# Kernel optimization log

Hardware: AMD Instinct MI355X
Metric: run time of the kernel (lower is better)

## Reference

```python
import jax, jax.numpy as jnp
import numpy as np

H = 4096      # hidden_size
Hk = 16       # num_key_heads
Dk = 256      # key_head_dim
Hv = 32       # num_value_heads
Dv = 256      # value_head_dim
G = 2         # kv_group_size
Ve = 512      # value_expand = G*Dv
CS = 4        # conv_size
QK = Hk * Dk  # 4096
VD = Hv * Dv  # 8192
EPS = 1e-6


def setup_inputs() -> dict:
    key = jax.random.key(0)
    ks = jax.random.split(key, 14)
    n = lambda i, shape, s: jax.random.normal(ks[i], shape, jnp.float32) * s
    return {
        "hidden_states": n(0, (1, H, 1, 1), 1.0),
        "Wq": n(1, (QK, H), 0.02),
        "Wk": n(2, (QK, H), 0.02),
        "Wv": n(3, (VD, H), 0.02),
        "Wo": n(4, (H, VD), 0.02),
        "Wa": n(5, (Hk, H), 0.02),
        "Wb": n(6, (Hk, H), 0.02),
        "q_conv_w": n(7, (1, QK, CS), 0.5),
        "k_conv_w": n(8, (1, QK, CS), 0.5),
        "v_conv_w": n(9, (1, VD, CS), 0.5),
        "q_cache": n(10, (1, QK, CS - 1), 1.0),
        "k_cache": n(11, (1, QK, CS - 1), 1.0),
        "v_cache": n(12, (1, VD, CS - 1), 1.0),
        "state": n(13, (1, Hk, Dk, Ve), 0.1),
    }


def _l2norm(x):
    return x * jax.lax.rsqrt(jnp.sum(x * x, axis=-1, keepdims=True) + EPS)


def reference(hidden_states, Wq, Wk, Wv, Wo, Wa, Wb,
              q_conv_w, k_conv_w, v_conv_w,
              q_cache, k_cache, v_cache, state):
    h = hidden_states[0, :, 0, 0]  # [H]
    q = Wq @ h                      # [QK]
    k = Wk @ h                      # [QK]
    v = Wv @ h                      # [VD]
    alpha = jax.nn.sigmoid(Wa @ h)  # [Hk]
    beta = jax.nn.sigmoid(Wb @ h)   # [Hk]

    # depthwise causal conv via cache concat + mul-sum, then SiLU
    q_full = jnp.concatenate([q_cache, q[None, :, None]], axis=2)  # [1,QK,CS]
    k_full = jnp.concatenate([k_cache, k[None, :, None]], axis=2)
    v_full = jnp.concatenate([v_cache, v[None, :, None]], axis=2)  # [1,VD,CS]
    q1 = jax.nn.silu(jnp.sum(q_full * q_conv_w, axis=2))  # [1,QK]
    k1 = jax.nn.silu(jnp.sum(k_full * k_conv_w, axis=2))
    v1 = jax.nn.silu(jnp.sum(v_full * v_conv_w, axis=2))  # [1,VD]

    q_heads = _l2norm(q1.reshape(1, Hk, Dk))
    k_heads = _l2norm(k1.reshape(1, Hk, Dk))
    v_heads = v1.reshape(1, Hk, Ve)  # Hv=Hk*G, Ve=G*Dv

    a = alpha.reshape(1, Hk, 1, 1)
    b = beta.reshape(1, Hk, 1, 1)
    state_decayed = state * a                                   # [1,Hk,Dk,Ve]
    retrieved = jnp.einsum('bhdv,bhd->bhv', state_decayed, k_heads)
    error = v_heads - retrieved                                 # [1,Hk,Ve]
    outer = k_heads[..., None] * error[:, :, None, :]           # [1,Hk,Dk,Ve]
    new_state = state_decayed + b * outer
    out = jnp.einsum('bhdv,bhd->bhv', new_state, q_heads)       # [1,Hk,Ve]
    out = out.reshape(1, VD)
    output = (out @ Wo.T).reshape(1, H, 1, 1)
    return output
```

## Files before the change

kernel.cpp:

```cpp
#include <hip/hip_runtime.h>
#include <math.h>

#define HDIM 4096
#define HK 16
#define DK 256
#define VE 512
#define QK 4096
#define VD 8192
#define NCHUNK 16
#define DPC 16
#define EPS 1e-6f

#define OFF_Q    0
#define OFF_K    4096
#define OFF_V    8192
#define OFF_AB   16384
#define OFF_KQ   16416
#define OFF_OUT  16432
#define OFF_PQ   24624
#define OFF_PK   (24624 + NCHUNK*VD)

typedef float f4_t __attribute__((ext_vector_type(4)));

__device__ __forceinline__ float sigmoidf_(float x) { return 1.f / (1.f + __expf(-x)); }
__device__ __forceinline__ float siluf_(float x)    { return x / (1.f + __expf(-x)); }

__global__ __launch_bounds__(256) void k1_gemv_all(
    const float* __restrict__ hvec,
    const float* __restrict__ Wq, const float* __restrict__ Wk,
    const float* __restrict__ Wv, const float* __restrict__ Wa,
    const float* __restrict__ Wb, float* __restrict__ ws) {
  int tid = threadIdx.x;
  int wave = tid >> 6, lane = tid & 63;
  int row = blockIdx.x * 4 + wave;
  if (row >= 16416) return;

  const f4_t* w4; float* outp;
  if (row < 4096)       { w4 = (const f4_t*)(Wq + (size_t)row * HDIM);            outp = ws + OFF_Q + row; }
  else if (row < 8192)  { int r = row - 4096;  w4 = (const f4_t*)(Wk + (size_t)r * HDIM); outp = ws + OFF_K + r; }
  else if (row < 16384) { int r = row - 8192;  w4 = (const f4_t*)(Wv + (size_t)r * HDIM); outp = ws + OFF_V + r; }
  else if (row < 16400) { int r = row - 16384; w4 = (const f4_t*)(Wa + (size_t)r * HDIM); outp = ws + OFF_AB + r; }
  else                  { int r = row - 16400; w4 = (const f4_t*)(Wb + (size_t)r * HDIM); outp = ws + OFF_AB + 16 + r; }

  const f4_t* h4 = (const f4_t*)hvec;
  float acc = 0.f;
#pragma unroll
  for (int j = 0; j < 16; ++j) {
    f4_t w  = __builtin_nontemporal_load(&w4[j * 64 + lane]);
    f4_t hv = h4[j * 64 + lane];
    acc += w.x * hv.x + w.y * hv.y + w.z * hv.z + w.w * hv.w;
  }
#pragma unroll
  for (int off = 32; off; off >>= 1) acc += __shfl_xor(acc, off, 64);
  if (lane == 0) *outp = acc;
}

__global__ __launch_bounds__(512) void kB_state(
    const float* __restrict__ qcw, const float* __restrict__ kcw,
    const float* __restrict__ qc,  const float* __restrict__ kc,
    const float* __restrict__ state, float* __restrict__ ws) {
  int hh = blockIdx.x >> 4;
  int c  = blockIdx.x & 15;
  int tid = threadIdx.x;
  __shared__ float q1s[DK], k1s[DK];
  __shared__ float red[3][8];

  float a = 0.f, b = 0.f, cc = 0.f;
  if (tid < DK) {
    int i = hh * DK + tid;
    float q1 = qc[i*3+0]*qcw[i*4+0] + qc[i*3+1]*qcw[i*4+1] + qc[i*3+2]*qcw[i*4+2]
             + ws[OFF_Q + i]*qcw[i*4+3];
    q1 = siluf_(q1);
    float k1 = kc[i*3+0]*kcw[i*4+0] + kc[i*3+1]*kcw[i*4+1] + kc[i*3+2]*kcw[i*4+2]
             + ws[OFF_K + i]*kcw[i*4+3];
    k1 = siluf_(k1);
    q1s[tid] = q1; k1s[tid] = k1;
    a = q1 * q1; b = k1 * k1; cc = q1 * k1;
  }
#pragma unroll
  for (int off = 32; off; off >>= 1) {
    a  += __shfl_xor(a, off, 64);
    b  += __shfl_xor(b, off, 64);
    cc += __shfl_xor(cc, off, 64);
  }
  int wave = tid >> 6, lane = tid & 63;
  if (lane == 0) { red[0][wave] = a; red[1][wave] = b; red[2][wave] = cc; }
  __syncthreads();
  float ssq = 0.f, ssk = 0.f, skq = 0.f;
#pragma unroll
  for (int w = 0; w < 8; ++w) { ssq += red[0][w]; ssk += red[1][w]; skq += red[2][w]; }
  float rq = rsqrtf(ssq + EPS), rk = rsqrtf(ssk + EPS);
  if (c == 0 && tid == 0) ws[OFF_KQ + hh] = skq * rq * rk;

  int vv = tid;
  int d0 = c * DPC;
  float aq = 0.f, ak = 0.f;
#pragma unroll
  for (int t = 0; t < DPC; ++t) {
    int d = d0 + t;
    float s = __builtin_nontemporal_load(state + ((size_t)(hh * DK + d)) * VE + vv);
    aq += s * q1s[d];
    ak += s * k1s[d];
  }
  ws[OFF_PQ + c * VD + hh * VE + vv] = aq * rq;
  ws[OFF_PK + c * VD + hh * VE + vv] = ak * rk;
}

__global__ __launch_bounds__(128) void kC_combine(
    const float* __restrict__ vcw, const float* __restrict__ vc,
    float* __restrict__ ws) {
  int hh = blockIdx.x >> 2;
  int vv = (blockIdx.x & 3) * 128 + threadIdx.x;
  int col = hh * VE + vv;

  float Sq = 0.f, Sk = 0.f;
#pragma unroll
  for (int c = 0; c < NCHUNK; ++c) {
    Sq += ws[OFF_PQ + c * VD + col];
    Sk += ws[OFF_PK + c * VD + col];
  }
  float v1 = vc[col*3+0]*vcw[col*4+0] + vc[col*3+1]*vcw[col*4+1] + vc[col*3+2]*vcw[col*4+2]
           + ws[OFF_V + col]*vcw[col*4+3];
  float vh = siluf_(v1);
  float a  = sigmoidf_(ws[OFF_AB + hh]);
  float bb = sigmoidf_(ws[OFF_AB + 16 + hh]);
  float kq = ws[OFF_KQ + hh];
  ws[OFF_OUT + col] = a * Sq + bb * kq * (vh - a * Sk);
}

__global__ __launch_bounds__(256) void kD_gemv_out(
    const float* __restrict__ Wo, const float* __restrict__ ws,
    float* __restrict__ dout) {
  int tid = threadIdx.x;
  int wave = tid >> 6, lane = tid & 63;
  int row = blockIdx.x * 4 + wave;
  const f4_t* r4 = (const f4_t*)(Wo + (size_t)row * VD);
  const f4_t* o4 = (const f4_t*)(ws + OFF_OUT);

  float acc = 0.f;
#pragma unroll
  for (int j = 0; j < 32; ++j) {
    f4_t w  = __builtin_nontemporal_load(&r4[j * 64 + lane]);
    f4_t ov = o4[j * 64 + lane];
    acc += w.x * ov.x + w.y * ov.y + w.z * ov.z + w.w * ov.w;
  }
#pragma unroll
  for (int off = 32; off; off >>= 1) acc += __shfl_xor(acc, off, 64);
  if (lane == 0) dout[row] = acc;
}

extern "C" void kernel_launch(void* const* d_in, const int* in_sizes, int n_in,
                              void* d_out, int out_size, void* d_ws, size_t ws_size,
                              hipStream_t stream) {
  const float* hvec = (const float*)d_in[0];
  const float* Wq   = (const float*)d_in[1];
  const float* Wk   = (const float*)d_in[2];
  const float* Wv   = (const float*)d_in[3];
  const float* Wo   = (const float*)d_in[4];
  const float* Wa   = (const float*)d_in[5];
  const float* Wb   = (const float*)d_in[6];
  const float* qcw  = (const float*)d_in[7];
  const float* kcw  = (const float*)d_in[8];
  const float* vcw  = (const float*)d_in[9];
  const float* qc   = (const float*)d_in[10];
  const float* kc   = (const float*)d_in[11];
  const float* vc   = (const float*)d_in[12];
  const float* state= (const float*)d_in[13];
  float* ws  = (float*)d_ws;
  float* out = (float*)d_out;

  k1_gemv_all<<<4104, 256, 0, stream>>>(hvec, Wq, Wk, Wv, Wa, Wb, ws);
  kB_state<<<256, 512, 0, stream>>>(qcw, kcw, qc, kc, state, ws);
  kC_combine<<<64, 128, 0, stream>>>(vcw, vc, ws);
  kD_gemv_out<<<1024, 256, 0, stream>>>(Wo, ws, out);
}
```

Baseline: 73.85 us.

## Fuse combine kernel into state kernel via last-block atomic counter

Removes the separate combine launch by having each state block bump an atomic counter after writing its partials; the last block to arrive then performs the chunk reduction and output mixing for all 8192 columns. The counter is reset in the first GEMV kernel. The change also drops the nontemporal hint on the first GEMV's weight loads. It saves one launch and gap, but the final combine now runs serially in a single 512-thread block and adds a fence and an atomic to every block.

```diff
diff --git a/kernel.cpp b/kernel.cpp
--- a/kernel.cpp
+++ b/kernel.cpp
@@ -5,7 +5,6 @@
 #define HK 16
 #define DK 256
 #define VE 512
-#define QK 4096
 #define VD 8192
 #define NCHUNK 16
 #define DPC 16
@@ -19,6 +18,7 @@
 #define OFF_OUT  16432
 #define OFF_PQ   24624
 #define OFF_PK   (24624 + NCHUNK*VD)
+#define OFF_CNT  (OFF_PK + NCHUNK*VD)
 
 typedef float f4_t __attribute__((ext_vector_type(4)));
 
@@ -30,6 +30,8 @@
     const float* __restrict__ Wq, const float* __restrict__ Wk,
     const float* __restrict__ Wv, const float* __restrict__ Wa,
     const float* __restrict__ Wb, float* __restrict__ ws) {
+  if (blockIdx.x == 0 && threadIdx.x == 0) *(int*)(ws + OFF_CNT) = 0;
+
   int tid = threadIdx.x;
   int wave = tid >> 6, lane = tid & 63;
   int row = blockIdx.x * 4 + wave;
@@ -46,7 +48,7 @@
   float acc = 0.f;
 #pragma unroll
   for (int j = 0; j < 16; ++j) {
-    f4_t w  = __builtin_nontemporal_load(&w4[j * 64 + lane]);
+    f4_t w  = w4[j * 64 + lane];
     f4_t hv = h4[j * 64 + lane];
     acc += w.x * hv.x + w.y * hv.y + w.z * hv.z + w.w * hv.w;
   }
@@ -58,12 +60,14 @@
 __global__ __launch_bounds__(512) void kB_state(
     const float* __restrict__ qcw, const float* __restrict__ kcw,
     const float* __restrict__ qc,  const float* __restrict__ kc,
+    const float* __restrict__ vcw, const float* __restrict__ vc,
     const float* __restrict__ state, float* __restrict__ ws) {
   int hh = blockIdx.x >> 4;
   int c  = blockIdx.x & 15;
   int tid = threadIdx.x;
   __shared__ float q1s[DK], k1s[DK];
   __shared__ float red[3][8];
+  __shared__ int lastFlag;
 
   float a = 0.f, b = 0.f, cc = 0.f;
   if (tid < DK) {
@@ -104,28 +108,32 @@
   }
   ws[OFF_PQ + c * VD + hh * VE + vv] = aq * rq;
   ws[OFF_PK + c * VD + hh * VE + vv] = ak * rk;
-}
 
-__global__ __launch_bounds__(128) void kC_combine(
-    const float* __restrict__ vcw, const float* __restrict__ vc,
-    float* __restrict__ ws) {
-  int hh = blockIdx.x >> 2;
-  int vv = (blockIdx.x & 3) * 128 + threadIdx.x;
-  int col = hh * VE + vv;
+  __threadfence();
+  if (tid == 0) {
+    int old = atomicAdd((int*)(ws + OFF_CNT), 1);
+    lastFlag = (old == 255);
+  }
+  __syncthreads();
+  if (!lastFlag) return;
+  __threadfence();
 
-  float Sq = 0.f, Sk = 0.f;
+  for (int col = tid; col < VD; col += 512) {
+    float Sq = 0.f, Sk = 0.f;
 #pragma unroll
-  for (int c = 0; c < NCHUNK; ++c) {
-    Sq += ws[OFF_PQ + c * VD + col];
-    Sk += ws[OFF_PK + c * VD + col];
+    for (int cch = 0; cch < NCHUNK; ++cch) {
+      Sq += ws[OFF_PQ + cch * VD + col];
+      Sk += ws[OFF_PK + cch * VD + col];
+    }
+    int h2 = col >> 9;
+    float v1 = vc[col*3+0]*vcw[col*4+0] + vc[col*3+1]*vcw[col*4+1] + vc[col*3+2]*vcw[col*4+2]
+             + ws[OFF_V + col]*vcw[col*4+3];
+    float vh  = siluf_(v1);
+    float aa  = sigmoidf_(ws[OFF_AB + h2]);
+    float bb  = sigmoidf_(ws[OFF_AB + 16 + h2]);
+    float kq  = ws[OFF_KQ + h2];
+    ws[OFF_OUT + col] = aa * Sq + bb * kq * (vh - aa * Sk);
   }
-  float v1 = vc[col*3+0]*vcw[col*4+0] + vc[col*3+1]*vcw[col*4+1] + vc[col*3+2]*vcw[col*4+2]
-           + ws[OFF_V + col]*vcw[col*4+3];
-  float vh = siluf_(v1);
-  float a  = sigmoidf_(ws[OFF_AB + hh]);
-  float bb = sigmoidf_(ws[OFF_AB + 16 + hh]);
-  float kq = ws[OFF_KQ + hh];
-  ws[OFF_OUT + col] = a * Sq + bb * kq * (vh - a * Sk);
 }
 
 __global__ __launch_bounds__(256) void kD_gemv_out(
@@ -170,7 +178,6 @@
   float* out = (float*)d_out;
 
   k1_gemv_all<<<4104, 256, 0, stream>>>(hvec, Wq, Wk, Wv, Wa, Wb, ws);
-  kB_state<<<256, 512, 0, stream>>>(qcw, kcw, qc, kc, state, ws);
-  kC_combine<<<64, 128, 0, stream>>>(vcw, vc, ws);
+  kB_state<<<256, 512, 0, stream>>>(qcw, kcw, qc, kc, vcw, vc, state, ws);
   kD_gemv_out<<<1024, 256, 0, stream>>>(Wo, ws, out);
 }
```

Result: slower. 136.1 us (+84.3%).
